# Kernel optimization log

Hardware: AMD Instinct MI355X
Metric: run time of the kernel (lower is better)

## Reference

```python
import jax, jax.numpy as jnp
import numpy as np

RES = 128
STEPSIZE = 0.5
NEAR, FAR, BG = 0.2, 3.0, 1.0
ALPHA_INIT = 0.01
XYZ_MIN, XYZ_MAX = -1.0, 1.0
N_RAYS = 1024
RGB_LATENT = 15
MULTIRES = 6
EMB_DIM = 3 + 3 * 2 * MULTIRES  # 39
DIM0 = RGB_LATENT + EMB_DIM     # 54
VOXEL = (XYZ_MAX - XYZ_MIN) / RES  # ((2^3)/RES^3)^(1/3)
N_SAMPLES = int(np.linalg.norm(np.array([RES] * 3) * 2 + 1) / STEPSIZE) + 1  # 891
ACT_SHIFT = float(np.log(1.0 / (1.0 - ALPHA_INIT) - 1.0))


def embed_dirs(d):
    # NeRF positional encoding, include_inputs=True, multires=6 -> 39 dims
    freqs = 2.0 ** jnp.arange(MULTIRES, dtype=d.dtype)
    ang = d[..., None, :] * freqs[:, None]  # [M,6,3]
    return jnp.concatenate([d, jnp.sin(ang).reshape(d.shape[0], -1), jnp.cos(ang).reshape(d.shape[0], -1)], -1)


def grid_sample3d(g, coords):
    # g: [C,D,H,W]; coords: [M,3] in (-1,1), torch grid_sample convention
    # (comp0 -> W axis, comp1 -> H axis, comp2 -> D axis), align_corners=True,
    # border-clamped indices (sampled out-of-box points are masked out anyway).
    C, D, H, W = g.shape
    x = (coords[:, 0] + 1) * 0.5 * (W - 1)
    y = (coords[:, 1] + 1) * 0.5 * (H - 1)
    z = (coords[:, 2] + 1) * 0.5 * (D - 1)
    x0, y0, z0 = jnp.floor(x), jnp.floor(y), jnp.floor(z)
    fx, fy, fz = x - x0, y - y0, z - z0
    x0i = jnp.clip(x0.astype(jnp.int32), 0, W - 1); x1i = jnp.clip(x0i + 1, 0, W - 1)
    y0i = jnp.clip(y0.astype(jnp.int32), 0, H - 1); y1i = jnp.clip(y0i + 1, 0, H - 1)
    z0i = jnp.clip(z0.astype(jnp.int32), 0, D - 1); z1i = jnp.clip(z0i + 1, 0, D - 1)
    gf = g.reshape(C, -1)
    def gv(zi, yi, xi):
        return gf[:, (zi * H + yi) * W + xi]  # [C,M]
    c = (((gv(z0i, y0i, x0i) * (1 - fx) + gv(z0i, y0i, x1i) * fx) * (1 - fy)
          + (gv(z0i, y1i, x0i) * (1 - fx) + gv(z0i, y1i, x1i) * fx) * fy) * (1 - fz)
         + ((gv(z1i, y0i, x0i) * (1 - fx) + gv(z1i, y0i, x1i) * fx) * (1 - fy)
            + (gv(z1i, y1i, x0i) * (1 - fx) + gv(z1i, y1i, x1i) * fx) * fy) * fz)
    return c.T  # [M,C]


def _forward(rays_o, rays_d, viewdirs, grid, sobel_kernel, w0, b0, w1, b1, w2, b2, w3, b3):
    # --- sample_ray: ray/AABB intersection + uniform stepping ---
    vec = jnp.where(rays_d == 0, 1e-6, rays_d)
    rate_a = (XYZ_MAX - rays_o) / vec
    rate_b = (XYZ_MIN - rays_o) / vec
    t_min = jnp.clip(jnp.minimum(rate_a, rate_b).max(-1), NEAR, FAR)
    t_max = jnp.clip(jnp.maximum(rate_a, rate_b).min(-1), NEAR, FAR)
    mask_ray = t_max <= t_min
    rng = jnp.arange(N_SAMPLES, dtype=rays_o.dtype)[None]
    step = STEPSIZE * VOXEL * rng
    interpx = t_min[:, None] + step / jnp.linalg.norm(rays_d, axis=-1, keepdims=True)
    pts = rays_o[:, None, :] + rays_d[:, None, :] * interpx[..., None]  # [N,S,3]
    inbox = (~mask_ray[:, None]) & (~((pts < XYZ_MIN) | (pts > XYZ_MAX)).any(-1))
    mflat = inbox.reshape(-1)

    # --- sobel normals grid (GridReg.forward(calc_normals=True)) ---
    density_grid = grid[None, :1]  # [1,1,D,H,W]
    nrm = jax.lax.conv_general_dilated(density_grid, sobel_kernel, (1, 1, 1), [(2, 2)] * 3,
                                       dimension_numbers=('NCDHW', 'OIDHW', 'NCDHW'))  # [1,3,D,H,W]
    nrm = -nrm / jnp.maximum(jnp.linalg.norm(nrm, axis=1, keepdims=True), 1e-12)
    normals_grid = nrm[0]

    # --- extract_latent: trilinear sample at ray points (masked via where) ---
    flat = pts.reshape(-1, 3)
    coords = ((flat - XYZ_MIN) / (XYZ_MAX - XYZ_MIN))[:, ::-1] * 2 - 1  # flip xyz->zyx
    lat = grid_sample3d(grid, coords)          # [M,16]
    ns = grid_sample3d(normals_grid, coords)   # [M,3]
    ns = -ns / jnp.maximum(jnp.linalg.norm(ns, axis=-1, keepdims=True), 1e-12)

    alpha = jnp.where(mflat, 1 - jnp.exp(-jax.nn.softplus(lat[:, 0] + ACT_SHIFT) * STEPSIZE), 0.0)
    alpha = alpha.reshape(N_RAYS, N_SAMPLES)
    normals = jnp.where(mflat[:, None], ns, 0.0).reshape(N_RAYS, N_SAMPLES, 3)
    rgb_lat = jnp.where(mflat[:, None], lat[:, 1:], 0.0)  # [M,15]

    # --- alpha compositing (cumprod_exclusive / get_ray_marching_ray) ---
    alphainv_cum = jnp.concatenate([jnp.ones_like(alpha[:, :1]),
                                    jnp.cumprod(jnp.maximum(1 - alpha, 1e-10), -1)], -1)
    weights = alpha * alphainv_cum[:, :-1]

    # --- reflected-direction shading MLP ---
    v = jnp.broadcast_to(viewdirs[:, None, :], normals.shape)
    dot = jnp.sum(-v * normals, -1, keepdims=True)
    refdirs = (2 * dot * normals + v).reshape(-1, 3)
    feat = jnp.concatenate([rgb_lat, embed_dirs(refdirs)], -1)  # [M,54]
    h = jax.nn.relu(feat @ w0 + b0)
    h = jax.nn.relu(h @ w1 + b1)
    h = jax.nn.relu(h @ w2 + b2)
    col = jax.nn.sigmoid(h @ w3 + b3)
    rgb = jnp.where(mflat[:, None], col, 0.0).reshape(N_RAYS, N_SAMPLES, 3)

    rgb_marched = (weights[..., None] * rgb).sum(-2) + alphainv_cum[:, -1:] * BG
    return rgb_marched


def setup_inputs() -> dict:
    key = jax.random.key(0)
    ks = jax.random.split(key, 8)
    rays_o = 0.3 * jax.random.normal(ks[0], (N_RAYS, 3), jnp.float32)
    rd = jax.random.normal(ks[1], (N_RAYS, 3), jnp.float32)
    rays_d = rd / jnp.linalg.norm(rd, axis=-1, keepdims=True)
    grid = 0.1 * jax.random.normal(ks[2], (1 + RGB_LATENT, RES, RES, RES), jnp.float32)
    sobel_kernel = jax.random.normal(ks[3], (3, 1, 5, 5, 5), jnp.float32)
    def lin(k, i, o):
        return jax.random.normal(k, (i, o), jnp.float32) / np.sqrt(i).astype(np.float32)
    return {
        'rays_o': rays_o, 'rays_d': rays_d, 'viewdirs': rays_d,
        'grid': grid, 'sobel_kernel': sobel_kernel,
        'w0': lin(ks[4], DIM0, 64), 'b0': jnp.zeros((64,), jnp.float32),
        'w1': lin(ks[5], 64, 64), 'b1': jnp.zeros((64,), jnp.float32),
        'w2': lin(ks[6], 64, 64), 'b2': jnp.zeros((64,), jnp.float32),
        'w3': lin(ks[7], 64, 3), 'b3': jnp.zeros((3,), jnp.float32),
    }


def reference(rays_o, rays_d, viewdirs, grid, sobel_kernel, w0, b0, w1, b1, w2, b2, w3, b3):
    return _forward(rays_o, rays_d, viewdirs, grid, sobel_kernel, w0, b0, w1, b1, w2, b2, w3, b3)
```

## Files before the change

kernel.cpp:

```cpp
#include <hip/hip_runtime.h>
#include <hip/hip_bf16.h>
#include <hip/hip_fp16.h>
#include <math.h>

#define RESV 128
#define V3 (RESV*RESV*RESV)
#define N_RAYS 1024
#define N_SAMPLES 891
#define STEP_T 0.0078125f
#define ACT_SHIFT -4.595119850134589f

typedef short bf16x8 __attribute__((ext_vector_type(8)));
typedef float f32x4 __attribute__((ext_vector_type(4)));

__device__ __forceinline__ unsigned short f2b(float x) {
    unsigned int u = __float_as_uint(x);
    unsigned int r = (u + 0x7FFFu + ((u >> 16) & 1u)) >> 16;
    return (unsigned short)r;
}

__device__ __forceinline__ void acc2(float w, unsigned int u, float& lo, float& hi) {
    lo = fmaf(w, __uint_as_float(u << 16), lo);
    hi = fmaf(w, __uint_as_float(u & 0xffff0000u), hi);
}

#define ROWS 60
#define ZSTR 136

template <bool PL>
__global__ __launch_bounds__(256)
void prep_kernel(const float* __restrict__ grid,
                 const float* __restrict__ sobel,
                 float4* __restrict__ nrm4,
                 unsigned short* __restrict__ latp,
                 const float* __restrict__ w0, const float* __restrict__ w1,
                 const float* __restrict__ w2, const float* __restrict__ w3,
                 unsigned short* __restrict__ wfr) {
    __shared__ float sk[375];
    __shared__ __align__(16) float tile[ROWS * ZSTR];

    const int t = threadIdx.x;
    const int bx = blockIdx.x;
    const int ix = bx >> 4;
    const int iy0 = (bx & 15) * 8;

    if (bx == 0) {
        for (int i = t; i < 26 * 64 * 8; i += 256) {
            const int j = i & 7;
            const int lane = (i >> 3) & 63;
            const int frag = i >> 9;
            const int r16 = lane & 15, q = lane >> 4;
            float v;
            if (frag < 24) {
                const int l = frag >> 3, ks = (frag >> 2) & 1, nb = frag & 3;
                const int n = nb * 16 + r16;
                const int k = ks * 32 + q * 8 + j;
                const float* W = (l == 0) ? w0 : (l == 1) ? w1 : w2;
                v = (l == 0 && k >= 54) ? 0.f : W[k * 64 + n];
            } else {
                const int ks = frag - 24;
                const int k = ks * 32 + q * 8 + j;
                v = (r16 < 3) ? w3[k * 3 + r16] : 0.f;
            }
            wfr[i] = f2b(v);
        }
    }

    for (int i = t; i < 375; i += 256) sk[i] = sobel[i];

    {
        const int lane32 = t & 31;
        for (int r = t >> 5; r < ROWS; r += 8) {
            const int xl = r / 12, yl = r % 12;
            const int gx = ix + xl - 2;
            const int gy = iy0 + yl - 2;
            float4 v = make_float4(0.f, 0.f, 0.f, 0.f);
            if ((unsigned)gx < 128u && (unsigned)gy < 128u)
                v = *(const float4*)&grid[(size_t)(gx * 128 + gy) * 128 + lane32 * 4];
            *(float4*)&tile[r * ZSTR + 4 + lane32 * 4] = v;
        }
        if (t < ROWS) {
            float* row = tile + t * ZSTR;
            row[0] = 0.f; row[1] = 0.f; row[2] = 0.f; row[3] = 0.f;
            row[132] = 0.f; row[133] = 0.f; row[134] = 0.f; row[135] = 0.f;
        }
    }
    __syncthreads();

    const int iz4 = (t & 31) * 4;
    const int iyl = t >> 5;
    const int vbase = (ix * 128 + iy0 + iyl) * 128 + iz4;

    float c0[4] = {0.f, 0.f, 0.f, 0.f};
    float c1[4] = {0.f, 0.f, 0.f, 0.f};
    float c2[4] = {0.f, 0.f, 0.f, 0.f};

    #pragma unroll
    for (int da = 0; da < 5; ++da) {
        #pragma unroll
        for (int db = 0; db < 5; ++db) {
            const float* row = tile + (da * 12 + iyl + db + 2) * ZSTR;
            const float* k0  = sk + (da * 5 + db) * 5;
            float gbuf[12];
            *(float4*)&gbuf[0] = *(const float4*)&row[iz4];
            *(float4*)&gbuf[4] = *(const float4*)&row[iz4 + 4];
            *(float4*)&gbuf[8] = *(const float4*)&row[iz4 + 8];
            #pragma unroll
            for (int zz = 0; zz < 4; ++zz) {
                #pragma unroll
                for (int dc = 0; dc < 5; ++dc) {
                    const float gv = gbuf[2 + zz + dc];
                    c0[zz] = fmaf(gv, k0[dc],       c0[zz]);
                    c1[zz] = fmaf(gv, k0[125 + dc], c1[zz]);
                    c2[zz] = fmaf(gv, k0[250 + dc], c2[zz]);
                }
            }
        }
    }
    #pragma unroll
    for (int zz = 0; zz < 4; ++zz) {
        float l   = sqrtf(c0[zz]*c0[zz] + c1[zz]*c1[zz] + c2[zz]*c2[zz]);
        float inv = -1.0f / fmaxf(l, 1e-12f);
        nrm4[vbase + zz] = make_float4(c0[zz]*inv, c1[zz]*inv, c2[zz]*inv, 0.f);
    }

    if constexpr (PL) {
        unsigned int r[4][8];
        #pragma unroll
        for (int c = 0; c < 16; c += 2) {
            const float4 a = *(const float4*)&grid[(size_t)c * V3 + vbase];
            const float4 b = *(const float4*)&grid[(size_t)(c + 1) * V3 + vbase];
            const float* pa = &a.x; const float* pb = &b.x;
            #pragma unroll
            for (int z = 0; z < 4; ++z)
                r[z][c >> 1] = (unsigned int)f2b(pa[z]) | ((unsigned int)f2b(pb[z]) << 16);
        }
        uint4* d = (uint4*)&latp[(size_t)vbase * 16];
        #pragma unroll
        for (int z = 0; z < 4; ++z) {
            d[z * 2 + 0] = make_uint4(r[z][0], r[z][1], r[z][2], r[z][3]);
            d[z * 2 + 1] = make_uint4(r[z][4], r[z][5], r[z][6], r[z][7]);
        }
    }
}

__device__ __forceinline__ void mfma_layer(unsigned short* __restrict__ actw,
                                           const unsigned short* __restrict__ wfr,
                                           int l, const float* __restrict__ Bv,
                                           int lane, int r16, int q4, int q8) {
    f32x4 acc[4][4];
    #pragma unroll
    for (int nb = 0; nb < 4; ++nb) {
        const float bv = Bv[nb * 16 + r16];
        #pragma unroll
        for (int mb = 0; mb < 4; ++mb) {
            acc[mb][nb][0] = bv; acc[mb][nb][1] = bv;
            acc[mb][nb][2] = bv; acc[mb][nb][3] = bv;
        }
    }
    #pragma unroll
    for (int ks = 0; ks < 2; ++ks) {
        bf16x8 Af[4], Bf[4];
        #pragma unroll
        for (int mb = 0; mb < 4; ++mb)
            Af[mb] = *(const bf16x8*)&actw[(mb * 16 + r16) * 72 + ks * 32 + q8];
        #pragma unroll
        for (int nb = 0; nb < 4; ++nb)
            Bf[nb] = *(const bf16x8*)&wfr[(size_t)((((l * 2 + ks) * 4) + nb) * 64 + lane) * 8];
        #pragma unroll
        for (int mb = 0; mb < 4; ++mb) {
            #pragma unroll
            for (int nb = 0; nb < 4; ++nb)
                acc[mb][nb] = __builtin_amdgcn_mfma_f32_16x16x32_bf16(
                    Af[mb], Bf[nb], acc[mb][nb], 0, 0, 0);
        }
    }
    #pragma unroll
    for (int mb = 0; mb < 4; ++mb) {
        #pragma unroll
        for (int nb = 0; nb < 4; ++nb) {
            #pragma unroll
            for (int r = 0; r < 4; ++r) {
                const int row = mb * 16 + q4 + r;
                actw[row * 72 + nb * 16 + r16] = f2b(fmaxf(acc[mb][nb][r], 0.f));
            }
        }
    }
}

template <bool PL>
__global__ __launch_bounds__(256, 3)
void raymarch_kernel(const float* __restrict__ ro, const float* __restrict__ rd,
                     const float* __restrict__ vd, const float* __restrict__ grid,
                     const float4* __restrict__ nrm4,
                     const unsigned short* __restrict__ latp,
                     const unsigned short* __restrict__ wfr,
                     const float* __restrict__ b0, const float* __restrict__ b1,
                     const float* __restrict__ b2, const float* __restrict__ b3,
                     float* __restrict__ out) {
    __shared__ __align__(16) unsigned short act[4 * 64 * 72];
    __shared__ float sb0f[64], sb1f[64], sb2f[64], sb3f[16];
    __shared__ __half salpha[1024];
    __shared__ __half scr[1024], scg[1024], scb[1024];
    __shared__ float lgl[1024];
    __shared__ float aux[256];
    __shared__ float red[12];

    const int t = threadIdx.x;
    const int ray = blockIdx.x;
    const int lane = t & 63;
    const int wave = t >> 6;
    const int r16 = lane & 15;
    const int q4 = (lane >> 4) * 4;
    const int q8 = (lane >> 4) * 8;
    unsigned short* const actw = act + wave * 64 * 72;

    if (t < 64) { sb0f[t] = b0[t]; sb1f[t] = b1[t]; sb2f[t] = b2[t]; }
    if (t < 16) sb3f[t] = (t < 3) ? b3[t] : 0.f;
    __syncthreads();

    const float ox = ro[ray * 3 + 0], oy = ro[ray * 3 + 1], oz = ro[ray * 3 + 2];
    const float dx = rd[ray * 3 + 0], dyv = rd[ray * 3 + 1], dzv = rd[ray * 3 + 2];
    const float vx = vd[ray * 3 + 0], vy = vd[ray * 3 + 1], vz = vd[ray * 3 + 2];

    const float ex = (dx  == 0.f) ? 1e-6f : dx;
    const float ey = (dyv == 0.f) ? 1e-6f : dyv;
    const float ez = (dzv == 0.f) ? 1e-6f : dzv;
    const float rax = (1.f - ox) / ex, rbx = (-1.f - ox) / ex;
    const float ray_ = (1.f - oy) / ey, rby = (-1.f - oy) / ey;
    const float raz = (1.f - oz) / ez, rbz = (-1.f - oz) / ez;
    float tmin = fmaxf(fmaxf(fminf(rax, rbx), fminf(ray_, rby)), fminf(raz, rbz));
    float tmax = fminf(fminf(fmaxf(rax, rbx), fmaxf(ray_, rby)), fmaxf(raz, rbz));
    tmin = fminf(fmaxf(tmin, 0.2f), 3.0f);
    tmax = fminf(fmaxf(tmax, 0.2f), 3.0f);
    const bool mask_ray = (tmax <= tmin);
    const float invn = 1.0f / sqrtf(dx * dx + dyv * dyv + dzv * dzv);

    #pragma unroll 1
    for (int j = 0; j < 4; ++j) {
        const int s = j * 256 + t;
        float alpha_s = 0.f;
        bool active = (s < N_SAMPLES) && !mask_ray;
        float px = 0.f, py = 0.f, pz = 0.f;
        if (active) {
            const float ti = tmin + STEP_T * (float)s * invn;
            px = fmaf(dx, ti, ox);
            py = fmaf(dyv, ti, oy);
            pz = fmaf(dzv, ti, oz);
            active = !(px < -1.f || px > 1.f || py < -1.f || py > 1.f ||
                       pz < -1.f || pz > 1.f);
        }
        const unsigned long long wmask = __ballot(active);
        if (wmask == 0ull) {
            salpha[s] = __float2half(0.f);
            lgl[s] = 0.f;
            scr[s] = __float2half(0.f); scg[s] = __float2half(0.f);
            scb[s] = __float2half(0.f);
            continue;
        }

        float feat[54];
        #pragma unroll
        for (int i = 0; i < 54; ++i) feat[i] = 0.f;

        if (active) {
            const float ga = (px + 1.f) * 63.5f;
            const float gb = (py + 1.f) * 63.5f;
            const float gc = (pz + 1.f) * 63.5f;
            const float fla = floorf(ga), flb = floorf(gb), flc = floorf(gc);
            const float fa = ga - fla, fb = gb - flb, fc = gc - flc;
            int ia0 = min(max((int)fla, 0), 127);
            int ib0 = min(max((int)flb, 0), 127);
            int ic0 = min(max((int)flc, 0), 127);
            int ia1 = min(ia0 + 1, 127);
            int ib1 = min(ib0 + 1, 127);
            int ic1 = min(ic0 + 1, 127);
            const int base00 = (ia0 * 128 + ib0) * 128;
            const int base01 = (ia0 * 128 + ib1) * 128;
            const int base10 = (ia1 * 128 + ib0) * 128;
            const int base11 = (ia1 * 128 + ib1) * 128;
            int idxs[8] = { base00 + ic0, base00 + ic1, base01 + ic0, base01 + ic1,
                            base10 + ic0, base10 + ic1, base11 + ic0, base11 + ic1 };
            const float wa0 = 1.f - fa, wb0 = 1.f - fb, wc0 = 1.f - fc;
            float w8[8] = { wa0*wb0*wc0, wa0*wb0*fc, wa0*fb*wc0, wa0*fb*fc,
                            fa*wb0*wc0,  fa*wb0*fc,  fa*fb*wc0,  fa*fb*fc };

            float lat[16];
            #pragma unroll
            for (int c = 0; c < 16; ++c) lat[c] = 0.f;
            if constexpr (PL) {
                #pragma unroll
                for (int k = 0; k < 8; ++k) {
                    const uint4* rec = (const uint4*)&latp[(size_t)idxs[k] * 16];
                    const uint4 u0 = rec[0];
                    const uint4 u1 = rec[1];
                    const float w = w8[k];
                    acc2(w, u0.x, lat[0],  lat[1]);
                    acc2(w, u0.y, lat[2],  lat[3]);
                    acc2(w, u0.z, lat[4],  lat[5]);
                    acc2(w, u0.w, lat[6],  lat[7]);
                    acc2(w, u1.x, lat[8],  lat[9]);
                    acc2(w, u1.y, lat[10], lat[11]);
                    acc2(w, u1.z, lat[12], lat[13]);
                    acc2(w, u1.w, lat[14], lat[15]);
                }
            } else {
                #pragma unroll
                for (int c = 0; c < 16; ++c) {
                    const float* gcp = grid + (size_t)c * V3;
                    float acc = 0.f;
                    #pragma unroll
                    for (int k = 0; k < 8; ++k) acc = fmaf(w8[k], gcp[idxs[k]], acc);
                    lat[c] = acc;
                }
            }
            const float lat0 = lat[0];
            #pragma unroll
            for (int c = 0; c < 15; ++c) feat[c] = lat[c + 1];

            float n0 = 0.f, n1 = 0.f, n2 = 0.f;
            #pragma unroll
            for (int k = 0; k < 8; ++k) {
                const float4 nv = nrm4[idxs[k]];
                n0 = fmaf(w8[k], nv.x, n0);
                n1 = fmaf(w8[k], nv.y, n1);
                n2 = fmaf(w8[k], nv.z, n2);
            }
            const float nl = sqrtf(n0*n0 + n1*n1 + n2*n2);
            const float ninv = -1.0f / fmaxf(nl, 1e-12f);
            n0 *= ninv; n1 *= ninv; n2 *= ninv;
            const float dotv = -(vx * n0 + vy * n1 + vz * n2);
            const float rx = fmaf(2.f * dotv, n0, vx);
            const float ry = fmaf(2.f * dotv, n1, vy);
            const float rz = fmaf(2.f * dotv, n2, vz);

            const float d0 = lat0 + ACT_SHIFT;
            const float sp = (d0 > 20.f) ? d0 : __logf(1.f + __expf(d0));
            alpha_s = 1.f - __expf(-sp * 0.5f);

            feat[15] = rx; feat[16] = ry; feat[17] = rz;
            float fr = 1.f;
            #pragma unroll
            for (int k = 0; k < 6; ++k) {
                feat[18 + k*3 + 0] = __sinf(rx * fr);
                feat[18 + k*3 + 1] = __sinf(ry * fr);
                feat[18 + k*3 + 2] = __sinf(rz * fr);
                feat[36 + k*3 + 0] = __cosf(rx * fr);
                feat[36 + k*3 + 1] = __cosf(ry * fr);
                feat[36 + k*3 + 2] = __cosf(rz * fr);
                fr *= 2.f;
            }
        }
        salpha[s] = __float2half(alpha_s);
        lgl[s] = __logf(fmaxf(1.f - alpha_s, 1e-10f));

        unsigned int* arow = (unsigned int*)&act[(size_t)t * 72];
        #pragma unroll
        for (int p = 0; p < 27; ++p)
            arow[p] = (unsigned int)f2b(feat[2*p]) |
                      ((unsigned int)f2b(feat[2*p + 1]) << 16);
        #pragma unroll
        for (int p = 27; p < 32; ++p) arow[p] = 0u;

        mfma_layer(actw, wfr, 0, sb0f, lane, r16, q4, q8);
        mfma_layer(actw, wfr, 1, sb1f, lane, r16, q4, q8);
        mfma_layer(actw, wfr, 2, sb2f, lane, r16, q4, q8);

        {
            f32x4 acch[4];
            const float bv = sb3f[r16];
            #pragma unroll
            for (int mb = 0; mb < 4; ++mb) {
                acch[mb][0] = bv; acch[mb][1] = bv;
                acch[mb][2] = bv; acch[mb][3] = bv;
            }
            #pragma unroll
            for (int ks = 0; ks < 2; ++ks) {
                const bf16x8 Bh = *(const bf16x8*)&wfr[(size_t)((24 + ks) * 64 + lane) * 8];
                #pragma unroll
                for (int mb = 0; mb < 4; ++mb) {
                    const bf16x8 Af = *(const bf16x8*)&actw[(mb * 16 + r16) * 72 + ks * 32 + q8];
                    acch[mb] = __builtin_amdgcn_mfma_f32_16x16x32_bf16(Af, Bh, acch[mb], 0, 0, 0);
                }
            }
            if (r16 < 3) {
                __half* dst = (r16 == 0) ? scr : (r16 == 1) ? scg : scb;
                const int jb = j * 256 + wave * 64;
                #pragma unroll
                for (int mb = 0; mb < 4; ++mb) {
                    #pragma unroll
                    for (int r = 0; r < 4; ++r) {
                        const int samp = mb * 16 + q4 + r;
                        dst[jb + samp] = __float2half(1.f / (1.f + __expf(-acch[mb][r])));
                    }
                }
            }
        }
    }
    __syncthreads();

    {
        float c0 = lgl[4*t + 0];
        float c1 = c0 + lgl[4*t + 1];
        float c2 = c1 + lgl[4*t + 2];
        float c3 = c2 + lgl[4*t + 3];
        lgl[4*t + 0] = c0; lgl[4*t + 1] = c1;
        lgl[4*t + 2] = c2; lgl[4*t + 3] = c3;
        aux[t] = c3;
    }
    __syncthreads();
    for (int off = 1; off < 256; off <<= 1) {
        const float v = (t >= off) ? aux[t - off] : 0.f;
        __syncthreads();
        aux[t] += v;
        __syncthreads();
    }
    const float total = aux[255];

    float r0 = 0.f, r1 = 0.f, r2 = 0.f;
    #pragma unroll
    for (int j = 0; j < 4; ++j) {
        const int s = j * 256 + t;
        const float a = __half2float(salpha[s]);
        if (s < N_SAMPLES && a > 0.f) {
            float G;
            if (s == 0) G = 0.f;
            else {
                const int m = s - 1;
                G = lgl[m] + (((m >> 2) > 0) ? aux[(m >> 2) - 1] : 0.f);
            }
            const float T = __expf(G);
            const float w = a * T;
            r0 = fmaf(w, __half2float(scr[s]), r0);
            r1 = fmaf(w, __half2float(scg[s]), r1);
            r2 = fmaf(w, __half2float(scb[s]), r2);
        }
    }
    #pragma unroll
    for (int off = 32; off > 0; off >>= 1) {
        r0 += __shfl_down(r0, off, 64);
        r1 += __shfl_down(r1, off, 64);
        r2 += __shfl_down(r2, off, 64);
    }
    if ((t & 63) == 0) {
        red[wave * 3 + 0] = r0; red[wave * 3 + 1] = r1; red[wave * 3 + 2] = r2;
    }
    __syncthreads();
    if (t == 0) {
        const float Tf = __expf(total);
        out[ray * 3 + 0] = red[0] + red[3] + red[6] + red[9]  + Tf;
        out[ray * 3 + 1] = red[1] + red[4] + red[7] + red[10] + Tf;
        out[ray * 3 + 2] = red[2] + red[5] + red[8] + red[11] + Tf;
    }
}

extern "C" void kernel_launch(void* const* d_in, const int* in_sizes, int n_in,
                              void* d_out, int out_size, void* d_ws, size_t ws_size,
                              hipStream_t stream) {
    (void)in_sizes; (void)n_in; (void)out_size;
    const float* ro    = (const float*)d_in[0];
    const float* rd    = (const float*)d_in[1];
    const float* vd    = (const float*)d_in[2];
    const float* grid  = (const float*)d_in[3];
    const float* sobel = (const float*)d_in[4];
    const float* w0 = (const float*)d_in[5];
    const float* b0 = (const float*)d_in[6];
    const float* w1 = (const float*)d_in[7];
    const float* b1 = (const float*)d_in[8];
    const float* w2 = (const float*)d_in[9];
    const float* b2 = (const float*)d_in[10];
    const float* w3 = (const float*)d_in[11];
    const float* b3 = (const float*)d_in[12];

    const size_t NRM_BYTES = (size_t)V3 * 16;
    const size_t LAT_BYTES = (size_t)V3 * 32;
    const size_t WFR_BYTES = 26 * 64 * 8 * 2;
    float4* nrm4 = (float4*)d_ws;
    const bool packed = (ws_size >= NRM_BYTES + LAT_BYTES + WFR_BYTES);
    unsigned short* latp = (unsigned short*)((char*)d_ws + NRM_BYTES);
    unsigned short* wfr  = packed
        ? (unsigned short*)((char*)d_ws + NRM_BYTES + LAT_BYTES)
        : (unsigned short*)((char*)d_ws + NRM_BYTES);

    if (packed) {
        prep_kernel<true><<<128 * 16, 256, 0, stream>>>(grid, sobel, nrm4, latp,
                                                        w0, w1, w2, w3, wfr);
        raymarch_kernel<true><<<N_RAYS, 256, 0, stream>>>(ro, rd, vd, grid, nrm4, latp, wfr,
                                                          b0, b1, b2, b3, (float*)d_out);
    } else {
        prep_kernel<false><<<128 * 16, 256, 0, stream>>>(grid, sobel, nrm4, latp,
                                                         w0, w1, w2, w3, wfr);
        raymarch_kernel<false><<<N_RAYS, 256, 0, stream>>>(ro, rd, vd, grid, nrm4, latp, wfr,
                                                           b0, b1, b2, b3, (float*)d_out);
    }
}
```

Before: 305.6 us.

## Retile sobel prep kernel into 16x64 y-z blocks with z halo

Changes the prep kernel's shared-memory tile from 8 y-rows by full z to 16 y-rows by a 64-wide z half, with explicit z halo loaded from global memory. This is meant to cut redundant y-halo loads per output voxel and keep each block's tile a similar size. In exchange, the x/y halo region gets larger and some extra z-halo rows are fetched. The 72-float row stride may also change the shared-memory bank-conflict behaviour.

```diff
diff --git a/kernel.cpp b/kernel.cpp
--- a/kernel.cpp
+++ b/kernel.cpp
@@ -24,8 +24,8 @@
     hi = fmaf(w, __uint_as_float(u & 0xffff0000u), hi);
 }
 
-#define ROWS 60
-#define ZSTR 136
+#define TROWS 100
+#define TZ 72
 
 template <bool PL>
 __global__ __launch_bounds__(256)
@@ -37,12 +37,15 @@
                  const float* __restrict__ w2, const float* __restrict__ w3,
                  unsigned short* __restrict__ wfr) {
     __shared__ float sk[375];
-    __shared__ __align__(16) float tile[ROWS * ZSTR];
+    __shared__ __align__(16) float tile[TROWS * TZ];
 
     const int t = threadIdx.x;
     const int bx = blockIdx.x;
     const int ix = bx >> 4;
-    const int iy0 = (bx & 15) * 8;
+    const int yt = (bx >> 1) & 7;
+    const int h  = bx & 1;
+    const int iy0 = yt * 16;
+    const int gz0 = h * 64;
 
     if (bx == 0) {
         for (int i = t; i < 26 * 64 * 8; i += 256) {
@@ -68,28 +71,25 @@
 
     for (int i = t; i < 375; i += 256) sk[i] = sobel[i];
 
-    {
-        const int lane32 = t & 31;
-        for (int r = t >> 5; r < ROWS; r += 8) {
-            const int xl = r / 12, yl = r % 12;
-            const int gx = ix + xl - 2;
-            const int gy = iy0 + yl - 2;
-            float4 v = make_float4(0.f, 0.f, 0.f, 0.f);
-            if ((unsigned)gx < 128u && (unsigned)gy < 128u)
-                v = *(const float4*)&grid[(size_t)(gx * 128 + gy) * 128 + lane32 * 4];
-            *(float4*)&tile[r * ZSTR + 4 + lane32 * 4] = v;
-        }
-        if (t < ROWS) {
-            float* row = tile + t * ZSTR;
-            row[0] = 0.f; row[1] = 0.f; row[2] = 0.f; row[3] = 0.f;
-            row[132] = 0.f; row[133] = 0.f; row[134] = 0.f; row[135] = 0.f;
-        }
+    for (int i = t; i < TROWS * 18; i += 256) {
+        const int r = i / 18;
+        const int c = i - r * 18;
+        const int xl = r / 20;
+        const int yl = r - xl * 20;
+        const int gx = ix + xl - 2;
+        const int gy = iy0 + yl - 2;
+        const int gz = gz0 - 4 + c * 4;
+        float4 v = make_float4(0.f, 0.f, 0.f, 0.f);
+        if ((unsigned)gx < 128u && (unsigned)gy < 128u && (unsigned)gz <= 124u)
+            v = *(const float4*)&grid[(size_t)(gx * 128 + gy) * 128 + gz];
+        *(float4*)&tile[r * TZ + c * 4] = v;
     }
     __syncthreads();
 
-    const int iz4 = (t & 31) * 4;
-    const int iyl = t >> 5;
-    const int vbase = (ix * 128 + iy0 + iyl) * 128 + iz4;
+    const int lz = t & 15;
+    const int ry = t >> 4;
+    const int iz4 = lz * 4;
+    const int vbase = (ix * 128 + iy0 + ry) * 128 + gz0 + iz4;
 
     float c0[4] = {0.f, 0.f, 0.f, 0.f};
     float c1[4] = {0.f, 0.f, 0.f, 0.f};
@@ -99,7 +99,7 @@
     for (int da = 0; da < 5; ++da) {
         #pragma unroll
         for (int db = 0; db < 5; ++db) {
-            const float* row = tile + (da * 12 + iyl + db + 2) * ZSTR;
+            const float* row = tile + (da * 20 + ry + db) * TZ;
             const float* k0  = sk + (da * 5 + db) * 5;
             float gbuf[12];
             *(float4*)&gbuf[0] = *(const float4*)&row[iz4];
@@ -483,13 +483,13 @@
         : (unsigned short*)((char*)d_ws + NRM_BYTES);
 
     if (packed) {
-        prep_kernel<true><<<128 * 16, 256, 0, stream>>>(grid, sobel, nrm4, latp,
-                                                        w0, w1, w2, w3, wfr);
+        prep_kernel<true><<<2048, 256, 0, stream>>>(grid, sobel, nrm4, latp,
+                                                    w0, w1, w2, w3, wfr);
         raymarch_kernel<true><<<N_RAYS, 256, 0, stream>>>(ro, rd, vd, grid, nrm4, latp, wfr,
                                                           b0, b1, b2, b3, (float*)d_out);
     } else {
-        prep_kernel<false><<<128 * 16, 256, 0, stream>>>(grid, sobel, nrm4, latp,
-                                                         w0, w1, w2, w3, wfr);
+        prep_kernel<false><<<2048, 256, 0, stream>>>(grid, sobel, nrm4, latp,
+                                                     w0, w1, w2, w3, wfr);
         raymarch_kernel<false><<<N_RAYS, 256, 0, stream>>>(ro, rd, vd, grid, nrm4, latp, wfr,
                                                            b0, b1, b2, b3, (float*)d_out);
     }
```

After: 313.8 us. +2.7%, slower.
